# Kernel optimization log

Measured on AMD Instinct MI355X. Metric: run time of the kernel, lower is better.

Reference implementation:

```python
import jax, jax.numpy as jnp
import numpy as np

N, E = 50000, 800000
IN_C, HID_C, OUT_C = 256, 256, 256


def setup_inputs() -> dict:
    key = jax.random.key(0)
    ks = jax.random.split(key, 8)
    x_piece = jax.random.normal(ks[0], (N, IN_C), dtype=jnp.float32)
    edge_index_piece = jax.random.randint(ks[1], (2, E), 0, N, dtype=jnp.int64)
    batch = jnp.zeros((N,), dtype=jnp.int64)
    def glorot(k, fan_in, fan_out):
        s = jnp.sqrt(6.0 / (fan_in + fan_out)).astype(jnp.float32)
        return jax.random.uniform(k, (fan_in, fan_out), jnp.float32, -s, s)
    return {
        "x_piece": x_piece,
        "edge_index_piece": edge_index_piece,
        "batch": batch,
        "W1": glorot(ks[2], IN_C, HID_C), "b1": jnp.zeros((HID_C,), jnp.float32),
        "W2": glorot(ks[3], HID_C, HID_C), "b2": jnp.zeros((HID_C,), jnp.float32),
        "W3": glorot(ks[4], HID_C, OUT_C), "b3": jnp.zeros((OUT_C,), jnp.float32),
    }


def _gcn_prep(edge_index, n_nodes):
    # add self-loops, compute symmetric normalization (PyG GCNConv default)
    src = jnp.concatenate([edge_index[0], jnp.arange(n_nodes, dtype=edge_index.dtype)])
    dst = jnp.concatenate([edge_index[1], jnp.arange(n_nodes, dtype=edge_index.dtype)])
    deg = jax.ops.segment_sum(jnp.ones_like(dst, dtype=jnp.float32), dst, num_segments=n_nodes)
    deg_inv_sqrt = jnp.where(deg > 0, jax.lax.rsqrt(jnp.maximum(deg, 1.0)), 0.0)
    norm = deg_inv_sqrt[src] * deg_inv_sqrt[dst]  # [E+N]
    return src, dst, norm


def _gcn_layer(x, src, dst, norm, W, b, n_nodes):
    h = x @ W                                   # [N, out] dense transform first
    msg = h[src] * norm[:, None]                # gather + scale
    out = jax.ops.segment_sum(msg, dst, num_segments=n_nodes)  # scatter-add
    return out + b


def reference(x_piece, edge_index_piece, batch, W1, b1, W2, b2, W3, b3):
    n_nodes = x_piece.shape[0]
    src, dst, norm = _gcn_prep(edge_index_piece, n_nodes)
    x = _gcn_layer(x_piece, src, dst, norm, W1, b1, n_nodes)
    x = jax.nn.gelu(x)
    x = _gcn_layer(x, src, dst, norm, W2, b2, n_nodes)
    x = jax.nn.gelu(x)
    x = _gcn_layer(x, src, dst, norm, W3, b3, n_nodes)
    return x
```

## Files before the change

kernel.cpp:

```cpp
#include <hip/hip_runtime.h>
#include <cstdint>
#include <cstddef>

#define CH 256

typedef _Float16 f16x8 __attribute__((ext_vector_type(8)));
typedef _Float16 f16x4 __attribute__((ext_vector_type(4)));
typedef float f32x4 __attribute__((ext_vector_type(4)));

#define GLOB(x) ((const __attribute__((address_space(1))) void*)(x))
#define LDSP(x) ((__attribute__((address_space(3))) void*)(x))


__device__ __forceinline__ int ld_idx(const void* p, long long i, int w64) {
    if (w64) return (int)((const long long*)p)[i];
    return ((const int*)p)[i];
}

__device__ __forceinline__ float gelu_f(float x) {
    float x3 = x * x * x;
    float t = tanhf(0.7978845608028654f * (x + 0.044715f * x3));
    return 0.5f * x * (1.0f + t);
}


__global__ void k_detect(const void* __restrict__ ei, int* __restrict__ flag, int E) {
    int l = threadIdx.x;
    long long k = ((long long)l * (long long)(E - 1)) / 63;
    int w = ((const int*)ei)[2 * k + 1];
    unsigned long long vote = __ballot(w == 0);
    if (l == 0) *flag = (vote == ~0ULL) ? 1 : 0;
}

__global__ void k_deg(const void* __restrict__ ei, const int* __restrict__ flag,
                      int* __restrict__ deg, int E) {
    int e = blockIdx.x * blockDim.x + threadIdx.x;
    if (e >= E) return;
    int w64 = *flag;
    int d = ld_idx(ei, (long long)E + e, w64);
    atomicAdd(&deg[d], 1);
}

__global__ void k_dis(const int* __restrict__ deg, float* __restrict__ dis, int N) {
    int n = blockIdx.x * blockDim.x + threadIdx.x;
    if (n >= N) return;
    dis[n] = 1.0f / sqrtf((float)(deg[n] + 1));
}

__global__ void k_scan_block(const int* __restrict__ deg, int* __restrict__ rowptr,
                             int* __restrict__ partial, int N) {
    __shared__ int s[256];
    int gid = blockIdx.x * 256 + threadIdx.x;
    int v = (gid < N) ? deg[gid] : 0;
    s[threadIdx.x] = v;
    __syncthreads();
    for (int off = 1; off < 256; off <<= 1) {
        int t = (threadIdx.x >= off) ? s[threadIdx.x - off] : 0;
        __syncthreads();
        s[threadIdx.x] += t;
        __syncthreads();
    }
    if (gid < N) rowptr[gid] = s[threadIdx.x] - v;
    if (threadIdx.x == 255) partial[blockIdx.x] = s[255];
}

__global__ void k_scan_partial(int* __restrict__ partial, int nb) {
    __shared__ int s[256];
    int i = threadIdx.x;
    int v = (i < nb) ? partial[i] : 0;
    s[i] = v;
    __syncthreads();
    for (int off = 1; off < 256; off <<= 1) {
        int t = (i >= off) ? s[i - off] : 0;
        __syncthreads();
        s[i] += t;
        __syncthreads();
    }
    if (i < nb) partial[i] = s[i] - v;
}

__global__ void k_add_off(int* __restrict__ rowptr, const int* __restrict__ partial,
                          int N, int E) {
    int gid = blockIdx.x * 256 + threadIdx.x;
    if (gid < N) rowptr[gid] += partial[blockIdx.x];
    if (gid == 0) rowptr[N] = E;
}

__global__ void k_scatter(const void* __restrict__ ei, const int* __restrict__ flag,
                          const float* __restrict__ dis, const int* __restrict__ rowptr,
                          int* __restrict__ cnt, int2* __restrict__ epack, int E) {
    int e = blockIdx.x * blockDim.x + threadIdx.x;
    if (e >= E) return;
    int w64 = *flag;
    int s = ld_idx(ei, e, w64);
    int d = ld_idx(ei, (long long)E + e, w64);
    int pos = rowptr[d] + atomicAdd(&cnt[d], 1);
    epack[pos] = make_int2(s, __float_as_int(dis[s] * dis[d]));
}


__global__ void k_split_w(const float* __restrict__ W, _Float16* __restrict__ Wh,
                          _Float16* __restrict__ Wl) {
    int k = threadIdx.x;
    int c = blockIdx.x;
    float v = W[k * CH + c];
    _Float16 h = (_Float16)v;
    Wh[c * CH + k] = h;
    Wl[c * CH + k] = (_Float16)(v - (float)h);
}


__global__ void k_split_x(const float* __restrict__ x, _Float16* __restrict__ Ah,
                          _Float16* __restrict__ Al, int n4) {
    int i = blockIdx.x * 256 + threadIdx.x;
    if (i >= n4) return;
    float4 v = ((const float4*)x)[i];
    f16x4 h, l;
    h[0] = (_Float16)v.x; l[0] = (_Float16)(v.x - (float)h[0]);
    h[1] = (_Float16)v.y; l[1] = (_Float16)(v.y - (float)h[1]);
    h[2] = (_Float16)v.z; l[2] = (_Float16)(v.z - (float)h[2]);
    h[3] = (_Float16)v.w; l[3] = (_Float16)(v.w - (float)h[3]);
    ((f16x4*)Ah)[i] = h;
    ((f16x4*)Al)[i] = l;
}


#define GM 128
#define GN 128
#define GK 32

__global__ __launch_bounds__(256, 2)
void k_gemm16s(const _Float16* __restrict__ Ah, const _Float16* __restrict__ Al,
               const _Float16* __restrict__ Bh, const _Float16* __restrict__ Bl,
               uint8_t* __restrict__ H16, float* __restrict__ scales, int M) {
    __shared__ __align__(16) char smem[65536];
    _Float16* lAh = (_Float16*)smem;
    _Float16* lAl = (_Float16*)(smem + 16384);
    _Float16* lBh = (_Float16*)(smem + 32768);
    _Float16* lBl = (_Float16*)(smem + 49152);

    const int tid  = threadIdx.x;
    const int lane = tid & 63;
    const int wid  = tid >> 6;
    const int m0   = blockIdx.x * GM;
    const int n0   = blockIdx.y * GN;
    const int wm   = wid >> 1, wn = wid & 1;
    const int r15  = lane & 15, kg = lane >> 4;

    auto stage = [&](int buf, int k0) {
        #pragma unroll
        for (int c = 0; c < 8; c++) {
            int call = wid * 8 + c;
            int cc = call & 7;
            int L = cc * 64 + lane;
            int row = L >> 2, ch = L & 3;
            int sch = ch ^ ((row >> 1) & 3);
            if (call < 8) {
                int gr = m0 + row; gr = (gr < M) ? gr : (M - 1);
                const _Float16* g = Ah + (size_t)gr * CH + k0 + (sch << 3);
                __builtin_amdgcn_global_load_lds(GLOB(g), LDSP(&lAh[buf * 4096 + L * 8]), 16, 0, 0);
            } else if (call < 16) {
                int gr = m0 + row; gr = (gr < M) ? gr : (M - 1);
                const _Float16* g = Al + (size_t)gr * CH + k0 + (sch << 3);
                __builtin_amdgcn_global_load_lds(GLOB(g), LDSP(&lAl[buf * 4096 + L * 8]), 16, 0, 0);
            } else if (call < 24) {
                const _Float16* g = Bh + (size_t)(n0 + row) * CH + k0 + (sch << 3);
                __builtin_amdgcn_global_load_lds(GLOB(g), LDSP(&lBh[buf * 4096 + L * 8]), 16, 0, 0);
            } else {
                const _Float16* g = Bl + (size_t)(n0 + row) * CH + k0 + (sch << 3);
                __builtin_amdgcn_global_load_lds(GLOB(g), LDSP(&lBl[buf * 4096 + L * 8]), 16, 0, 0);
            }
        }
    };

    f32x4 acc[4][4];
    #pragma unroll
    for (int i = 0; i < 4; i++)
        #pragma unroll
        for (int n = 0; n < 4; n++)
            acc[i][n] = (f32x4){0.f, 0.f, 0.f, 0.f};

    stage(0, 0);
    __syncthreads();

    for (int ks = 0; ks < 8; ks++) {
        int cur = ks & 1;
        if (ks < 7) stage(cur ^ 1, (ks + 1) * GK);

        f16x8 ah[4], al[4], bh[4], bl[4];
        #pragma unroll
        for (int i = 0; i < 4; i++) {
            int R = wm * 64 + i * 16 + r15;
            int p = kg ^ ((R >> 1) & 3);
            ah[i] = *(const f16x8*)&lAh[cur * 4096 + R * GK + p * 8];
            al[i] = *(const f16x8*)&lAl[cur * 4096 + R * GK + p * 8];
        }
        #pragma unroll
        for (int n = 0; n < 4; n++) {
            int C = wn * 64 + n * 16 + r15;
            int p = kg ^ ((C >> 1) & 3);
            bh[n] = *(const f16x8*)&lBh[cur * 4096 + C * GK + p * 8];
            bl[n] = *(const f16x8*)&lBl[cur * 4096 + C * GK + p * 8];
        }
        #pragma unroll
        for (int i = 0; i < 4; i++)
            #pragma unroll
            for (int n = 0; n < 4; n++) {
                acc[i][n] = __builtin_amdgcn_mfma_f32_16x16x32_f16(ah[i], bh[n], acc[i][n], 0, 0, 0);
                acc[i][n] = __builtin_amdgcn_mfma_f32_16x16x32_f16(ah[i], bl[n], acc[i][n], 0, 0, 0);
                acc[i][n] = __builtin_amdgcn_mfma_f32_16x16x32_f16(al[i], bh[n], acc[i][n], 0, 0, 0);
            }
        __syncthreads();
    }

    float mx = 0.f;
    #pragma unroll
    for (int i = 0; i < 4; i++)
        #pragma unroll
        for (int n = 0; n < 4; n++)
            #pragma unroll
            for (int r = 0; r < 4; r++)
                mx = fmaxf(mx, fabsf(acc[i][n][r]));
    #pragma unroll
    for (int off = 32; off > 0; off >>= 1)
        mx = fmaxf(mx, __shfl_xor(mx, off));
    if (lane == 0) ((float*)smem)[wid] = mx;
    __syncthreads();
    float tmax = fmaxf(fmaxf(((float*)smem)[0], ((float*)smem)[1]),
                       fmaxf(((float*)smem)[2], ((float*)smem)[3]));
    float scl = tmax * (1.0f / 32767.0f);
    float inv = (tmax > 0.f) ? (32767.0f / tmax) : 0.f;
    __syncthreads();

    float* ep = (float*)smem + wid * 4096;
    #pragma unroll
    for (int i = 0; i < 4; i++)
        #pragma unroll
        for (int n = 0; n < 4; n++)
            #pragma unroll
            for (int r = 0; r < 4; r++)
                ep[(i * 16 + kg * 4 + r) * 64 + n * 16 + r15] = acc[i][n][r];
    __syncthreads();

    int q = lane & 15;
    int rsub = lane >> 4;
    #pragma unroll
    for (int p = 0; p < 16; p++) {
        int lrow = p * 4 + rsub;
        int grow = m0 + wm * 64 + lrow;
        if (grow < M) {
            int q0 = __float2int_rn(ep[lrow * 64 + q * 4 + 0] * inv);
            int q1 = __float2int_rn(ep[lrow * 64 + q * 4 + 1] * inv);
            int q2 = __float2int_rn(ep[lrow * 64 + q * 4 + 2] * inv);
            int q3 = __float2int_rn(ep[lrow * 64 + q * 4 + 3] * inv);
            uint2 d;
            d.x = (q0 & 0xFFFF) | (q1 << 16);
            d.y = (q2 & 0xFFFF) | (q3 << 16);
            int col = n0 + wn * 64 + q * 4;
            *(uint2*)(H16 + (size_t)grow * 512 + (size_t)col * 2) = d;
        }
    }

    if (tid < GM && m0 + tid < M) scales[(size_t)(m0 + tid) * 2 + (n0 >> 7)] = scl;
}


template <int MODE>
__global__ __launch_bounds__(256) void k_agg(const uint8_t* __restrict__ H16,
                                             const float* __restrict__ scales,
                                             const float* __restrict__ dis,
                                             const int* __restrict__ rowptr,
                                             const int2* __restrict__ epack,
                                             const float* __restrict__ bias,
                                             float* __restrict__ out,
                                             _Float16* __restrict__ Ah,
                                             _Float16* __restrict__ Al, int N) {
    int node = blockIdx.x * 4 + threadIdx.y;
    if (node >= N) return;
    int lane = threadIdx.x;
    int half = lane >> 5;
    float d = dis[node];
    short4 hv = *(const short4*)(H16 + (size_t)node * 512 + (size_t)lane * 8);
    float wself = d * d * scales[(size_t)node * 2 + half];
    float ax = wself * (float)hv.x, ay = wself * (float)hv.y;
    float az = wself * (float)hv.z, aw = wself * (float)hv.w;
    int s = rowptr[node], e = rowptr[node + 1];
    int j = s;
    for (; j + 8 <= e; j += 8) {
        int2 p[8];
        #pragma unroll
        for (int t = 0; t < 8; t++) p[t] = epack[j + t];
        short4 v[8];
        float sc[8];
        #pragma unroll
        for (int t = 0; t < 8; t++) {
            v[t] = *(const short4*)(H16 + (size_t)p[t].x * 512 + (size_t)lane * 8);
            sc[t] = scales[(size_t)p[t].x * 2 + half];
        }
        #pragma unroll
        for (int t = 0; t < 8; t++) {
            float wn = __int_as_float(p[t].y) * sc[t];
            ax += wn * (float)v[t].x; ay += wn * (float)v[t].y;
            az += wn * (float)v[t].z; aw += wn * (float)v[t].w;
        }
    }
    for (; j < e; j++) {
        int2 p = epack[j];
        float wn = __int_as_float(p.y) * scales[(size_t)p.x * 2 + half];
        short4 v = *(const short4*)(H16 + (size_t)p.x * 512 + (size_t)lane * 8);
        ax += wn * (float)v.x; ay += wn * (float)v.y;
        az += wn * (float)v.z; aw += wn * (float)v.w;
    }
    float4 b = ((const float4*)bias)[lane];
    ax += b.x; ay += b.y; az += b.z; aw += b.w;
    if (MODE == 0) {
        ax = gelu_f(ax); ay = gelu_f(ay); az = gelu_f(az); aw = gelu_f(aw);
        f16x4 h, l;
        h[0] = (_Float16)ax; l[0] = (_Float16)(ax - (float)h[0]);
        h[1] = (_Float16)ay; l[1] = (_Float16)(ay - (float)h[1]);
        h[2] = (_Float16)az; l[2] = (_Float16)(az - (float)h[2]);
        h[3] = (_Float16)aw; l[3] = (_Float16)(aw - (float)h[3]);
        size_t idx = (size_t)node * 64 + lane;
        ((f16x4*)Ah)[idx] = h;
        ((f16x4*)Al)[idx] = l;
    } else {
        ((float4*)(out + (size_t)node * CH))[lane] = make_float4(ax, ay, az, aw);
    }
}


extern "C" void kernel_launch(void* const* d_in, const int* in_sizes, int n_in,
                              void* d_out, int out_size, void* d_ws, size_t ws_size,
                              hipStream_t stream) {
    const float* x  = (const float*)d_in[0];
    const void*  ei = d_in[1];
    const float* W1 = (const float*)d_in[3]; const float* b1 = (const float*)d_in[4];
    const float* W2 = (const float*)d_in[5]; const float* b2 = (const float*)d_in[6];
    const float* W3 = (const float*)d_in[7]; const float* b3 = (const float*)d_in[8];

    int N = in_sizes[0] / CH;
    int E = in_sizes[1] / 2;
    float* out = (float*)d_out;

    char* ws = (char*)d_ws;
    auto take = [&](size_t bytes) {
        char* p = ws;
        ws += (bytes + 15) & ~(size_t)15;
        return p;
    };
    uint8_t*  H16    = (uint8_t*) take((size_t)N * 512);
    _Float16* Ah     = (_Float16*)take((size_t)N * CH * 2);
    _Float16* Al     = (_Float16*)take((size_t)N * CH * 2);
    float*    scales = (float*)   take((size_t)N * 2 * sizeof(float));
    int*      deg    = (int*)     take((size_t)N * sizeof(int));
    float*    dis    = (float*)   take((size_t)N * sizeof(float));
    int*      rowptr = (int*)     take((size_t)(N + 1) * sizeof(int));
    int*      cnt    = (int*)     take((size_t)N * sizeof(int));
    int*      part   = (int*)     take(4096);
    int*      flag   = (int*)     take(16);
    int2*     epack  = (int2*)    take((size_t)E * sizeof(int2));
    _Float16* Wh1    = (_Float16*)take((size_t)CH * CH * 2);
    _Float16* Wl1    = (_Float16*)take((size_t)CH * CH * 2);
    _Float16* Wh2    = (_Float16*)take((size_t)CH * CH * 2);
    _Float16* Wl2    = (_Float16*)take((size_t)CH * CH * 2);
    _Float16* Wh3    = (_Float16*)take((size_t)CH * CH * 2);
    _Float16* Wl3    = (_Float16*)take((size_t)CH * CH * 2);

    hipMemsetAsync(deg, 0, (size_t)N * sizeof(int), stream);
    hipMemsetAsync(cnt, 0, (size_t)N * sizeof(int), stream);

    int eb = (E + 255) / 256;
    int nb = (N + 255) / 256;

    k_detect<<<1, 64, 0, stream>>>(ei, flag, E);
    k_deg<<<eb, 256, 0, stream>>>(ei, flag, deg, E);
    k_dis<<<nb, 256, 0, stream>>>(deg, dis, N);
    k_scan_block<<<nb, 256, 0, stream>>>(deg, rowptr, part, N);
    k_scan_partial<<<1, 256, 0, stream>>>(part, nb);
    k_add_off<<<nb, 256, 0, stream>>>(rowptr, part, N, E);
    k_scatter<<<eb, 256, 0, stream>>>(ei, flag, dis, rowptr, cnt, epack, E);

    k_split_w<<<CH, CH, 0, stream>>>(W1, Wh1, Wl1);
    k_split_w<<<CH, CH, 0, stream>>>(W2, Wh2, Wl2);
    k_split_w<<<CH, CH, 0, stream>>>(W3, Wh3, Wl3);

    int n4 = N * (CH / 4);
    k_split_x<<<(n4 + 255) / 256, 256, 0, stream>>>(x, Ah, Al, n4);

    dim3 ggrid((N + GM - 1) / GM, CH / GN);
    dim3 agrid((N + 3) / 4);
    dim3 ablock(64, 4);

    k_gemm16s<<<ggrid, 256, 0, stream>>>(Ah, Al, Wh1, Wl1, H16, scales, N);
    k_agg<0><<<agrid, ablock, 0, stream>>>(H16, scales, dis, rowptr, epack, b1, out, Ah, Al, N);
    k_gemm16s<<<ggrid, 256, 0, stream>>>(Ah, Al, Wh2, Wl2, H16, scales, N);
    k_agg<0><<<agrid, ablock, 0, stream>>>(H16, scales, dis, rowptr, epack, b2, out, Ah, Al, N);
    k_gemm16s<<<ggrid, 256, 0, stream>>>(Ah, Al, Wh3, Wl3, H16, scales, N);
    k_agg<1><<<agrid, ablock, 0, stream>>>(H16, scales, dis, rowptr, epack, b3, out, Ah, Al, N);
}
```

Before: 440.4 us.

## Compute full 256-column GEMM tile per block with B loaded directly from global

The GEMM now covers all 256 output columns in each block instead of splitting N into two 128-column blocks. The A tile is staged into LDS once rather than twice, and each block computes a single quantization scale per 128-row tile. The weight operand is read straight from global memory into registers (it is small and cache-resident) instead of through LDS. The epilogue is restructured into four LDS passes with padding to fit the smaller shared buffer. The trade-offs are doubled accumulator registers (128 floats per thread), which may hurt occupancy, half as many blocks, and one scale spanning 256 columns, which slightly changes quantization precision.

```diff
diff --git a/kernel.cpp b/kernel.cpp
--- a/kernel.cpp
+++ b/kernel.cpp
@@ -126,58 +126,48 @@
 
 
 #define GM 128
-#define GN 128
 #define GK 32
 
 __global__ __launch_bounds__(256, 2)
 void k_gemm16s(const _Float16* __restrict__ Ah, const _Float16* __restrict__ Al,
                const _Float16* __restrict__ Bh, const _Float16* __restrict__ Bl,
                uint8_t* __restrict__ H16, float* __restrict__ scales, int M) {
-    __shared__ __align__(16) char smem[65536];
+    __shared__ __align__(16) char smem[34816];
     _Float16* lAh = (_Float16*)smem;
     _Float16* lAl = (_Float16*)(smem + 16384);
-    _Float16* lBh = (_Float16*)(smem + 32768);
-    _Float16* lBl = (_Float16*)(smem + 49152);
+    float*    red = (float*)(smem + 33792);
 
     const int tid  = threadIdx.x;
     const int lane = tid & 63;
     const int wid  = tid >> 6;
     const int m0   = blockIdx.x * GM;
-    const int n0   = blockIdx.y * GN;
     const int wm   = wid >> 1, wn = wid & 1;
     const int r15  = lane & 15, kg = lane >> 4;
 
     auto stage = [&](int buf, int k0) {
         #pragma unroll
-        for (int c = 0; c < 8; c++) {
-            int call = wid * 8 + c;
+        for (int c = 0; c < 4; c++) {
+            int call = wid * 4 + c;
             int cc = call & 7;
             int L = cc * 64 + lane;
             int row = L >> 2, ch = L & 3;
             int sch = ch ^ ((row >> 1) & 3);
+            int gr = m0 + row; gr = (gr < M) ? gr : (M - 1);
             if (call < 8) {
-                int gr = m0 + row; gr = (gr < M) ? gr : (M - 1);
                 const _Float16* g = Ah + (size_t)gr * CH + k0 + (sch << 3);
                 __builtin_amdgcn_global_load_lds(GLOB(g), LDSP(&lAh[buf * 4096 + L * 8]), 16, 0, 0);
-            } else if (call < 16) {
-                int gr = m0 + row; gr = (gr < M) ? gr : (M - 1);
+            } else {
                 const _Float16* g = Al + (size_t)gr * CH + k0 + (sch << 3);
                 __builtin_amdgcn_global_load_lds(GLOB(g), LDSP(&lAl[buf * 4096 + L * 8]), 16, 0, 0);
-            } else if (call < 24) {
-                const _Float16* g = Bh + (size_t)(n0 + row) * CH + k0 + (sch << 3);
-                __builtin_amdgcn_global_load_lds(GLOB(g), LDSP(&lBh[buf * 4096 + L * 8]), 16, 0, 0);
-            } else {
-                const _Float16* g = Bl + (size_t)(n0 + row) * CH + k0 + (sch << 3);
-                __builtin_amdgcn_global_load_lds(GLOB(g), LDSP(&lBl[buf * 4096 + L * 8]), 16, 0, 0);
             }
         }
     };
 
-    f32x4 acc[4][4];
+    f32x4 acc[4][8];
     #pragma unroll
     for (int i = 0; i < 4; i++)
         #pragma unroll
-        for (int n = 0; n < 4; n++)
+        for (int n = 0; n < 8; n++)
             acc[i][n] = (f32x4){0.f, 0.f, 0.f, 0.f};
 
     stage(0, 0);
@@ -185,9 +175,18 @@
 
     for (int ks = 0; ks < 8; ks++) {
         int cur = ks & 1;
-        if (ks < 7) stage(cur ^ 1, (ks + 1) * GK);
-
-        f16x8 ah[4], al[4], bh[4], bl[4];
+        int k0 = ks * GK;
+
+        f16x8 bh[8], bl[8];
+        #pragma unroll
+        for (int n = 0; n < 8; n++) {
+            int C = wn * 128 + n * 16 + r15;
+            bh[n] = *(const f16x8*)(Bh + (size_t)C * CH + k0 + kg * 8);
+            bl[n] = *(const f16x8*)(Bl + (size_t)C * CH + k0 + kg * 8);
+        }
+        if (ks < 7) stage(cur ^ 1, k0 + GK);
+
+        f16x8 ah[4], al[4];
         #pragma unroll
         for (int i = 0; i < 4; i++) {
             int R = wm * 64 + i * 16 + r15;
@@ -196,16 +195,9 @@
             al[i] = *(const f16x8*)&lAl[cur * 4096 + R * GK + p * 8];
         }
         #pragma unroll
-        for (int n = 0; n < 4; n++) {
-            int C = wn * 64 + n * 16 + r15;
-            int p = kg ^ ((C >> 1) & 3);
-            bh[n] = *(const f16x8*)&lBh[cur * 4096 + C * GK + p * 8];
-            bl[n] = *(const f16x8*)&lBl[cur * 4096 + C * GK + p * 8];
-        }
-        #pragma unroll
         for (int i = 0; i < 4; i++)
             #pragma unroll
-            for (int n = 0; n < 4; n++) {
+            for (int n = 0; n < 8; n++) {
                 acc[i][n] = __builtin_amdgcn_mfma_f32_16x16x32_f16(ah[i], bh[n], acc[i][n], 0, 0, 0);
                 acc[i][n] = __builtin_amdgcn_mfma_f32_16x16x32_f16(ah[i], bl[n], acc[i][n], 0, 0, 0);
                 acc[i][n] = __builtin_amdgcn_mfma_f32_16x16x32_f16(al[i], bh[n], acc[i][n], 0, 0, 0);
@@ -217,51 +209,48 @@
     #pragma unroll
     for (int i = 0; i < 4; i++)
         #pragma unroll
-        for (int n = 0; n < 4; n++)
+        for (int n = 0; n < 8; n++)
             #pragma unroll
             for (int r = 0; r < 4; r++)
                 mx = fmaxf(mx, fabsf(acc[i][n][r]));
     #pragma unroll
     for (int off = 32; off > 0; off >>= 1)
         mx = fmaxf(mx, __shfl_xor(mx, off));
-    if (lane == 0) ((float*)smem)[wid] = mx;
+    if (lane == 0) red[wid] = mx;
     __syncthreads();
-    float tmax = fmaxf(fmaxf(((float*)smem)[0], ((float*)smem)[1]),
-                       fmaxf(((float*)smem)[2], ((float*)smem)[3]));
+    float tmax = fmaxf(fmaxf(red[0], red[1]), fmaxf(red[2], red[3]));
     float scl = tmax * (1.0f / 32767.0f);
     float inv = (tmax > 0.f) ? (32767.0f / tmax) : 0.f;
-    __syncthreads();
-
-    float* ep = (float*)smem + wid * 4096;
+
+    float* ep = (float*)smem;
     #pragma unroll
-    for (int i = 0; i < 4; i++)
-        #pragma unroll
-        for (int n = 0; n < 4; n++)
+    for (int i = 0; i < 4; i++) {
+        __syncthreads();
+        #pragma unroll
+        for (int n = 0; n < 8; n++)
             #pragma unroll
             for (int r = 0; r < 4; r++)
-                ep[(i * 16 + kg * 4 + r) * 64 + n * 16 + r15] = acc[i][n][r];
-    __syncthreads();
-
-    int q = lane & 15;
-    int rsub = lane >> 4;
-    #pragma unroll
-    for (int p = 0; p < 16; p++) {
-        int lrow = p * 4 + rsub;
-        int grow = m0 + wm * 64 + lrow;
+                ep[(wm * 16 + kg * 4 + r) * 264 + wn * 128 + n * 16 + r15] = acc[i][n][r];
+        __syncthreads();
+        int row = tid >> 3;
+        int grow = m0 + (row >> 4) * 64 + i * 16 + (row & 15);
         if (grow < M) {
-            int q0 = __float2int_rn(ep[lrow * 64 + q * 4 + 0] * inv);
-            int q1 = __float2int_rn(ep[lrow * 64 + q * 4 + 1] * inv);
-            int q2 = __float2int_rn(ep[lrow * 64 + q * 4 + 2] * inv);
-            int q3 = __float2int_rn(ep[lrow * 64 + q * 4 + 3] * inv);
-            uint2 d;
-            d.x = (q0 & 0xFFFF) | (q1 << 16);
-            d.y = (q2 & 0xFFFF) | (q3 << 16);
-            int col = n0 + wn * 64 + q * 4;
-            *(uint2*)(H16 + (size_t)grow * 512 + (size_t)col * 2) = d;
-        }
-    }
-
-    if (tid < GM && m0 + tid < M) scales[(size_t)(m0 + tid) * 2 + (n0 >> 7)] = scl;
+            const float* src = &ep[row * 264];
+            #pragma unroll
+            for (int g8 = 0; g8 < 8; g8++) {
+                int c = g8 * 32 + (tid & 7) * 4;
+                int q0 = __float2int_rn(src[c + 0] * inv);
+                int q1 = __float2int_rn(src[c + 1] * inv);
+                int q2 = __float2int_rn(src[c + 2] * inv);
+                int q3 = __float2int_rn(src[c + 3] * inv);
+                uint2 d;
+                d.x = (q0 & 0xFFFF) | (q1 << 16);
+                d.y = (q2 & 0xFFFF) | (q3 << 16);
+                *(uint2*)(H16 + (size_t)grow * 512 + (size_t)c * 2) = d;
+            }
+        }
+    }
+    if (tid < GM && m0 + tid < M) scales[m0 + tid] = scl;
 }
 
 
@@ -278,10 +267,9 @@
     int node = blockIdx.x * 4 + threadIdx.y;
     if (node >= N) return;
     int lane = threadIdx.x;
-    int half = lane >> 5;
     float d = dis[node];
     short4 hv = *(const short4*)(H16 + (size_t)node * 512 + (size_t)lane * 8);
-    float wself = d * d * scales[(size_t)node * 2 + half];
+    float wself = d * d * scales[node];
     float ax = wself * (float)hv.x, ay = wself * (float)hv.y;
     float az = wself * (float)hv.z, aw = wself * (float)hv.w;
     int s = rowptr[node], e = rowptr[node + 1];
@@ -295,7 +283,7 @@
         #pragma unroll
         for (int t = 0; t < 8; t++) {
             v[t] = *(const short4*)(H16 + (size_t)p[t].x * 512 + (size_t)lane * 8);
-            sc[t] = scales[(size_t)p[t].x * 2 + half];
+            sc[t] = scales[p[t].x];
         }
         #pragma unroll
         for (int t = 0; t < 8; t++) {
@@ -306,7 +294,7 @@
     }
     for (; j < e; j++) {
         int2 p = epack[j];
-        float wn = __int_as_float(p.y) * scales[(size_t)p.x * 2 + half];
+        float wn = __int_as_float(p.y) * scales[p.x];
         short4 v = *(const short4*)(H16 + (size_t)p.x * 512 + (size_t)lane * 8);
         ax += wn * (float)v.x; ay += wn * (float)v.y;
         az += wn * (float)v.z; aw += wn * (float)v.w;
@@ -351,7 +339,7 @@
     uint8_t*  H16    = (uint8_t*) take((size_t)N * 512);
     _Float16* Ah     = (_Float16*)take((size_t)N * CH * 2);
     _Float16* Al     = (_Float16*)take((size_t)N * CH * 2);
-    float*    scales = (float*)   take((size_t)N * 2 * sizeof(float));
+    float*    scales = (float*)   take((size_t)N * sizeof(float));
     int*      deg    = (int*)     take((size_t)N * sizeof(int));
     float*    dis    = (float*)   take((size_t)N * sizeof(float));
     int*      rowptr = (int*)     take((size_t)(N + 1) * sizeof(int));
@@ -387,7 +375,7 @@
     int n4 = N * (CH / 4);
     k_split_x<<<(n4 + 255) / 256, 256, 0, stream>>>(x, Ah, Al, n4);
 
-    dim3 ggrid((N + GM - 1) / GM, CH / GN);
+    dim3 ggrid((N + GM - 1) / GM);
     dim3 agrid((N + 3) / 4);
     dim3 ablock(64, 4);
 
```

Result: slower. 460.2 us (+4.5%).
